# Kernel optimization log

Hardware: AMD Instinct MI355X
Metric: run time of the kernel (lower is better)

The kernel has to match this reference:

```python
import jax, jax.numpy as jnp
import numpy as np
import math

N_HEADS = 16
FACTOR = 5
EPS = 1e-5


def layernorm(x, g, b):
    m = x.mean(-1, keepdims=True)
    v = x.var(-1, keepdims=True)
    return (x - m) / jnp.sqrt(v + EPS) * g + b


def prob_attention(Q, K, V, mask_flag, key):
    # Q: [B, L_Q, H, D], K/V: [B, L_K, H, D] -> internal [B, H, L, D] (Informer ProbAttention)
    Q = Q.transpose(0, 2, 1, 3)
    K = K.transpose(0, 2, 1, 3)
    V = V.transpose(0, 2, 1, 3)
    B, H, L_Q, D = Q.shape
    L_K = K.shape[2]
    U_part = min(FACTOR * int(np.ceil(np.log(L_K))), L_K)  # sampled keys per query
    u = min(FACTOR * int(np.ceil(np.log(L_Q))), L_Q)       # number of active queries
    # sample U_part key indices per query (shared over B, H as in Informer)
    idx = jax.random.randint(key, (L_Q, U_part), 0, L_K)
    K_s = K[:, :, idx, :]                                   # [B,H,L_Q,U_part,D]
    QKs = jnp.einsum('bhld,bhlsd->bhls', Q, K_s)            # sampled scores
    M = QKs.max(-1) - QKs.sum(-1) / L_K                     # sparsity measurement [B,H,L_Q]
    M_top = jax.lax.top_k(M, u)[1]                          # [B,H,u] active query indices
    Q_r = jnp.take_along_axis(Q, M_top[..., None], axis=2)  # [B,H,u,D]
    scale = 1.0 / math.sqrt(D)
    scores = jnp.einsum('bhud,bhkd->bhuk', Q_r, K) * scale  # [B,H,u,L_K]
    if mask_flag:
        # causal mask relative to each selected query's position
        causal = jnp.arange(L_K)[None, None, None, :] > M_top[..., None]
        scores = jnp.where(causal, -jnp.inf, scores)
        context = jnp.cumsum(V, axis=2)                     # initial context for masked case
    else:
        context = jnp.broadcast_to(V.mean(axis=2, keepdims=True), (B, H, L_Q, D))
    attn = jax.nn.softmax(scores, axis=-1)
    ctx = jnp.einsum('bhuk,bhkd->bhud', attn, V)            # [B,H,u,D]
    bi = jnp.arange(B)[:, None, None]
    hi = jnp.arange(H)[None, :, None]
    context = context.at[bi, hi, M_top].set(ctx)            # scatter active queries
    return context.transpose(0, 2, 1, 3)                    # [B,L_Q,H,D]


def mha(x, kv, Wq, bq, Wk, bk, Wv, bv, Wo, bo, mask_flag, key):
    B, L, Dm = x.shape
    Lc = kv.shape[1]
    Dh = Dm // N_HEADS
    Q = (x @ Wq + bq).reshape(B, L, N_HEADS, Dh)
    K = (kv @ Wk + bk).reshape(B, Lc, N_HEADS, Dh)
    V = (kv @ Wv + bv).reshape(B, Lc, N_HEADS, Dh)
    out = prob_attention(Q, K, V, mask_flag, key).reshape(B, L, Dm)
    return out @ Wo + bo


def forward(x, enc_out, sa_Wq, sa_bq, sa_Wk, sa_bk, sa_Wv, sa_bv, sa_Wo, sa_bo,
            ca_Wq, ca_bq, ca_Wk, ca_bk, ca_Wv, ca_bv, ca_Wo, ca_bo,
            ln1_g, ln1_b, ln2_g, ln2_b, ln3_g, ln3_b, ff_W1, ff_b1, ff_W2, ff_b2):
    k1, k2 = jax.random.split(jax.random.key(42))
    x2 = mha(x, x, sa_Wq, sa_bq, sa_Wk, sa_bk, sa_Wv, sa_bv, sa_Wo, sa_bo, True, k1)
    x = layernorm(x + x2, ln1_g, ln1_b)
    x2 = mha(x, enc_out, ca_Wq, ca_bq, ca_Wk, ca_bk, ca_Wv, ca_bv, ca_Wo, ca_bo, False, k2)
    x = layernorm(x + x2, ln2_g, ln2_b)
    x2 = (jax.nn.relu(x @ ff_W1 + ff_b1)) @ ff_W2 + ff_b2
    return layernorm(x + x2, ln3_g, ln3_b)


def setup_inputs() -> dict:
    key = jax.random.key(0)
    D, F = 1024, 4096
    B, L = 4, 1024
    ks = jax.random.split(key, 16)
    s = 0.02
    inp = {
        'x': jax.random.normal(ks[0], (B, L, D), jnp.float32),
        'enc_out': jax.random.normal(ks[1], (B, L, D), jnp.float32),
    }
    names = ['sa_Wq', 'sa_Wk', 'sa_Wv', 'sa_Wo', 'ca_Wq', 'ca_Wk', 'ca_Wv', 'ca_Wo']
    for i, n in enumerate(names):
        inp[n] = jax.random.normal(ks[2 + i], (D, D), jnp.float32) * s
        inp[n.replace('W', 'b')] = jnp.zeros((D,), jnp.float32)
    inp['ff_W1'] = jax.random.normal(ks[10], (D, F), jnp.float32) * s
    inp['ff_b1'] = jnp.zeros((F,), jnp.float32)
    inp['ff_W2'] = jax.random.normal(ks[11], (F, D), jnp.float32) * s
    inp['ff_b2'] = jnp.zeros((D,), jnp.float32)
    for i in (1, 2, 3):
        inp[f'ln{i}_g'] = jnp.ones((D,), jnp.float32)
        inp[f'ln{i}_b'] = jnp.zeros((D,), jnp.float32)
    return inp


def reference(x, enc_out, sa_Wq, sa_bq, sa_Wk, sa_bk, sa_Wv, sa_bv, sa_Wo, sa_bo,
              ca_Wq, ca_bq, ca_Wk, ca_bk, ca_Wv, ca_bv, ca_Wo, ca_bo,
              ln1_g, ln1_b, ln2_g, ln2_b, ln3_g, ln3_b, ff_W1, ff_b1, ff_W2, ff_b2):
    return forward(x, enc_out, sa_Wq, sa_bq, sa_Wk, sa_bk, sa_Wv, sa_bv, sa_Wo, sa_bo,
                   ca_Wq, ca_bq, ca_Wk, ca_bk, ca_Wv, ca_bv, ca_Wo, ca_bo,
                   ln1_g, ln1_b, ln2_g, ln2_b, ln3_g, ln3_b, ff_W1, ff_b1, ff_W2, ff_b2)
```

## Files before the change

kernel.cpp:

```cpp
#include <hip/hip_runtime.h>
#include <cstdint>
#include <cstddef>

#define B_     4
#define L_     1024
#define DM_    1024
#define H_     16
#define DH_    64
#define U_     35
#define FF_    4096
#define MROWS_ 4096
#define IDXN_  35840
#define KS_    4
#define KSP_   16

typedef __attribute__((ext_vector_type(8))) short bf16x8;
typedef __attribute__((ext_vector_type(4))) float f32x4;

__host__ __device__ inline void tf2x32(uint32_t k0, uint32_t k1,
                                       uint32_t x0, uint32_t x1,
                                       uint32_t& y0, uint32_t& y1) {
  const uint32_t ks2 = k0 ^ k1 ^ 0x1BD11BDAu;
  uint32_t v0 = x0 + k0, v1 = x1 + k1;
#define ROTL_(x,d) (((x)<<(d))|((x)>>(32-(d))))
#define RND_(r) { v0 += v1; v1 = ROTL_(v1,(r)); v1 ^= v0; }
  RND_(13) RND_(15) RND_(26) RND_(6)   v0 += k1;  v1 += ks2 + 1u;
  RND_(17) RND_(29) RND_(16) RND_(24)  v0 += ks2; v1 += k0  + 2u;
  RND_(13) RND_(15) RND_(26) RND_(6)   v0 += k0;  v1 += k1  + 3u;
  RND_(17) RND_(29) RND_(16) RND_(24)  v0 += k1;  v1 += ks2 + 4u;
  RND_(13) RND_(15) RND_(26) RND_(6)   v0 += ks2; v1 += k0  + 5u;
#undef RND_
#undef ROTL_
  y0 = v0; y1 = v1;
}

__global__ void idx_kernel(uint32_t k0, uint32_t k1, int* __restrict__ idx) {
  const int i = blockIdx.x * 256 + threadIdx.x;
  if (i >= IDXN_) return;
  uint32_t y0, y1;
  tf2x32(k0, k1, 0u, (uint32_t)i, y0, y1);
  idx[i] = (int)((y0 ^ y1) & 1023u);
}

__device__ __forceinline__ uint32_t f32bits(float x) {
  union { float f; uint32_t u; } c; c.f = x; return c.u;
}
__device__ __forceinline__ float bitsf32(uint32_t u) {
  union { uint32_t u; float f; } c; c.u = u; return c.f;
}
__device__ __forceinline__ uint32_t bf16rne(float x) {
  const uint32_t u = f32bits(x);
  return (u + 0x7FFFu + ((u >> 16) & 1u)) >> 16;
}
__device__ __forceinline__ float bf16tof(uint32_t h) { return bitsf32(h << 16); }

__device__ __forceinline__ void split3(float x, uint32_t& h, uint32_t& m, uint32_t& l) {
  h = bf16rne(x); const float r  = x - bf16tof(h);
  m = bf16rne(r); const float r2 = r - bf16tof(m);
  l = bf16rne(r2);
}

__device__ __forceinline__ void gload16(const void* g, void* l) {
  __builtin_amdgcn_global_load_lds(
      (const __attribute__((address_space(1))) void*)g,
      (__attribute__((address_space(3))) void*)l, 16, 0, 0);
}

template<int LIMBS>
__global__ __launch_bounds__(256) void tsplit_kernel(
    const float* __restrict__ W, short* __restrict__ Th,
    short* __restrict__ Tm, short* __restrict__ Tl, int K, int N)
{
  __shared__ float tile[64][65];
  const int n0 = blockIdx.x * 64, k0 = blockIdx.y * 64;
  const int t = threadIdx.x;
  const int r = t >> 2, c0 = (t & 3) * 16;
  const float* src = W + (size_t)(k0 + r) * N + n0 + c0;
  const float4 v0 = *(const float4*)src;
  const float4 v1 = *(const float4*)(src + 4);
  const float4 v2 = *(const float4*)(src + 8);
  const float4 v3 = *(const float4*)(src + 12);
  float* tr = &tile[r][c0];
  tr[0]=v0.x; tr[1]=v0.y; tr[2]=v0.z; tr[3]=v0.w;
  tr[4]=v1.x; tr[5]=v1.y; tr[6]=v1.z; tr[7]=v1.w;
  tr[8]=v2.x; tr[9]=v2.y; tr[10]=v2.z; tr[11]=v2.w;
  tr[12]=v3.x; tr[13]=v3.y; tr[14]=v3.z; tr[15]=v3.w;
  __syncthreads();
  uint32_t ph[8], pm[8], pl[8];
#pragma unroll
  for (int j = 0; j < 16; j += 2) {
    uint32_t h0,m0,l0,h1,m1,l1;
    split3(tile[c0 + j][r], h0, m0, l0);
    split3(tile[c0 + j + 1][r], h1, m1, l1);
    ph[j>>1] = h0 | (h1 << 16);
    pm[j>>1] = m0 | (m1 << 16);
    pl[j>>1] = l0 | (l1 << 16);
  }
  const size_t ob = (size_t)(n0 + r) * K + k0 + c0;
  *(uint4*)(Th + ob)     = make_uint4(ph[0], ph[1], ph[2], ph[3]);
  *(uint4*)(Th + ob + 8) = make_uint4(ph[4], ph[5], ph[6], ph[7]);
  if (LIMBS == 3) {
    *(uint4*)(Tm + ob)     = make_uint4(pm[0], pm[1], pm[2], pm[3]);
    *(uint4*)(Tm + ob + 8) = make_uint4(pm[4], pm[5], pm[6], pm[7]);
    *(uint4*)(Tl + ob)     = make_uint4(pl[0], pl[1], pl[2], pl[3]);
    *(uint4*)(Tl + ob + 8) = make_uint4(pl[4], pl[5], pl[6], pl[7]);
  }
}

template<int LIMBS>
__global__ void rsplit_kernel(const float* __restrict__ X, short* __restrict__ Th,
                              short* __restrict__ Tm, short* __restrict__ Tl, int n8)
{
  const int i = blockIdx.x * 256 + threadIdx.x;
  if (i >= n8) return;
  const float4 a = ((const float4*)X)[2*i], b = ((const float4*)X)[2*i+1];
  const float v[8] = {a.x,a.y,a.z,a.w,b.x,b.y,b.z,b.w};
  uint32_t ph[4], pm[4], pl[4];
#pragma unroll
  for (int j = 0; j < 4; ++j) {
    uint32_t h0,m0,l0,h1,m1,l1;
    split3(v[2*j], h0, m0, l0);
    split3(v[2*j+1], h1, m1, l1);
    ph[j] = h0 | (h1 << 16); pm[j] = m0 | (m1 << 16); pl[j] = l0 | (l1 << 16);
  }
  ((uint4*)Th)[i] = make_uint4(ph[0], ph[1], ph[2], ph[3]);
  if (LIMBS == 3) {
    ((uint4*)Tm)[i] = make_uint4(pm[0], pm[1], pm[2], pm[3]);
    ((uint4*)Tl)[i] = make_uint4(pl[0], pl[1], pl[2], pl[3]);
  }
}

struct FJob {
  const short* A[3];
  const short* B[3];
  const float* bias;
  float* C;
  short* Ch;
  int relu;
};
struct FJobs { FJob j[3]; };

template<int NL>
__global__ __launch_bounds__(256, 2) void gemm_fused(FJobs jobs, int K, int N)
{
  __shared__ short As[NL][4096] __attribute__((aligned(16)));
  __shared__ short Bs[NL][4096] __attribute__((aligned(16)));
  const int z = blockIdx.z;
  const int nwg  = gridDim.x * gridDim.y;
  const int flat = blockIdx.y * gridDim.x + blockIdx.x;
  const int swz  = (flat & 7) * (nwg >> 3) + (flat >> 3);
  const int bn = (swz % gridDim.x) * 128;
  const int bm = (swz / gridDim.x) * 128;

  const int t = threadIdx.x, lane = t & 63;
  const int wid = t >> 6, wr = wid >> 1, wc = wid & 1;
  const int l15 = lane & 15, kg = lane >> 4;
  const int srow = t >> 2;
  const int sc   = ((t & 3) ^ ((srow + (srow >> 2)) & 3)) * 8;

  int aoff[4], boff[4];
#pragma unroll
  for (int m = 0; m < 4; ++m) {
    const int ra = wr * 64 + m * 16 + l15;
    aoff[m] = ra * 32 + ((kg ^ ((ra + (ra >> 2)) & 3)) << 3);
    const int rb = wc * 64 + m * 16 + l15;
    boff[m] = rb * 32 + ((kg ^ ((rb + (rb >> 2)) & 3)) << 3);
  }

  f32x4 acc[4][4];
#pragma unroll
  for (int m = 0; m < 4; ++m)
#pragma unroll
    for (int n = 0; n < 4; ++n) acc[m][n] = (f32x4){0.f,0.f,0.f,0.f};

  const size_t aofs0 = (size_t)(bm + srow) * K + sc;
  const size_t bofs0 = (size_t)(bn + srow) * K + sc;
  const size_t half  = (size_t)64 * K;

  for (int kk = 0; kk < K; kk += 32) {
    __syncthreads();
#pragma unroll
    for (int l = 0; l < NL; ++l) {
      gload16(jobs.j[z].A[l] + aofs0 + kk,        &As[l][t * 8]);
      gload16(jobs.j[z].A[l] + aofs0 + half + kk, &As[l][2048 + t * 8]);
      gload16(jobs.j[z].B[l] + bofs0 + kk,        &Bs[l][t * 8]);
      gload16(jobs.j[z].B[l] + bofs0 + half + kk, &Bs[l][2048 + t * 8]);
    }
    __syncthreads();
    if (NL == 1) {
      bf16x8 a[4], b[4];
#pragma unroll
      for (int m = 0; m < 4; ++m) a[m] = *(const bf16x8*)&As[0][aoff[m]];
#pragma unroll
      for (int n = 0; n < 4; ++n) b[n] = *(const bf16x8*)&Bs[0][boff[n]];
#pragma unroll
      for (int m = 0; m < 4; ++m)
#pragma unroll
        for (int n = 0; n < 4; ++n)
          acc[m][n] = __builtin_amdgcn_mfma_f32_16x16x32_bf16(a[m], b[n], acc[m][n], 0, 0, 0);
    } else {
      bf16x8 a0[4], a1[4], a2[4], b[4];
#pragma unroll
      for (int m = 0; m < 4; ++m) {
        a0[m] = *(const bf16x8*)&As[0][aoff[m]];
        a1[m] = *(const bf16x8*)&As[1][aoff[m]];
        a2[m] = *(const bf16x8*)&As[2][aoff[m]];
      }
#pragma unroll
      for (int n = 0; n < 4; ++n) b[n] = *(const bf16x8*)&Bs[0][boff[n]];
#pragma unroll
      for (int m = 0; m < 4; ++m)
#pragma unroll
        for (int n = 0; n < 4; ++n) {
          acc[m][n] = __builtin_amdgcn_mfma_f32_16x16x32_bf16(a0[m], b[n], acc[m][n], 0, 0, 0);
          acc[m][n] = __builtin_amdgcn_mfma_f32_16x16x32_bf16(a1[m], b[n], acc[m][n], 0, 0, 0);
          acc[m][n] = __builtin_amdgcn_mfma_f32_16x16x32_bf16(a2[m], b[n], acc[m][n], 0, 0, 0);
        }
#pragma unroll
      for (int n = 0; n < 4; ++n) b[n] = *(const bf16x8*)&Bs[1][boff[n]];
#pragma unroll
      for (int m = 0; m < 4; ++m)
#pragma unroll
        for (int n = 0; n < 4; ++n) {
          acc[m][n] = __builtin_amdgcn_mfma_f32_16x16x32_bf16(a0[m], b[n], acc[m][n], 0, 0, 0);
          acc[m][n] = __builtin_amdgcn_mfma_f32_16x16x32_bf16(a1[m], b[n], acc[m][n], 0, 0, 0);
        }
#pragma unroll
      for (int n = 0; n < 4; ++n) b[n] = *(const bf16x8*)&Bs[2][boff[n]];
#pragma unroll
      for (int m = 0; m < 4; ++m)
#pragma unroll
        for (int n = 0; n < 4; ++n)
          acc[m][n] = __builtin_amdgcn_mfma_f32_16x16x32_bf16(a0[m], b[n], acc[m][n], 0, 0, 0);
    }
  }

  const float* bias = jobs.j[z].bias;
  float* C  = jobs.j[z].C;
  short* Ch = jobs.j[z].Ch;
  const int relu = jobs.j[z].relu;
  float bv[4];
#pragma unroll
  for (int n = 0; n < 4; ++n) bv[n] = bias[bn + wc*64 + n*16 + l15];
#pragma unroll
  for (int m = 0; m < 4; ++m) {
    const int row0 = bm + wr*64 + m*16 + kg*4;
#pragma unroll
    for (int n = 0; n < 4; ++n) {
      const int col = bn + wc*64 + n*16 + l15;
#pragma unroll
      for (int q = 0; q < 4; ++q) {
        float o = acc[m][n][q] + bv[n];
        if (relu) o = fmaxf(o, 0.f);
        const size_t off = (size_t)(row0 + q) * N + col;
        if (C)  C[off]  = o;
        if (Ch) Ch[off] = (short)bf16rne(o);
      }
    }
  }
}

__global__ __launch_bounds__(256, 2) void qks_m_kernel(
    const float* __restrict__ Q, const float* __restrict__ K,
    const int* __restrict__ idx, float* __restrict__ Mout)
{
  __shared__ int sidx[64 * U_];
  const int p = blockIdx.x;
  const int g  = (p & 7) + (((p >> 3) & 7) << 3);
  const int q16 = p >> 6;
  const int l0 = q16 * 64;
  const int tid = threadIdx.x;
  for (int i = tid; i < 64 * U_; i += 256) sidx[i] = idx[l0 * U_ + i];
  __syncthreads();

  const int ll = tid >> 2, dq = tid & 3;
  const int l = l0 + ll;
  const int h = g & (H_ - 1), b = g >> 4;
  const size_t rowb = (size_t)(b * L_) * DM_ + h * DH_;
  const float* qrow = Q + rowb + (size_t)l * DM_ + dq * 4;
  float4 qv[4];
#pragma unroll
  for (int jj = 0; jj < 4; ++jj) qv[jj] = *(const float4*)(qrow + jj * 16);

  const int* ip = &sidx[ll * U_];
  float mx = -__builtin_inff();
  float sm = 0.f;
#pragma unroll 5
  for (int s = 0; s < U_; ++s) {
    const float* krow = K + rowb + (size_t)ip[s] * DM_ + dq * 4;
    const float4 k0 = *(const float4*)(krow);
    const float4 k1 = *(const float4*)(krow + 16);
    const float4 k2 = *(const float4*)(krow + 32);
    const float4 k3 = *(const float4*)(krow + 48);
    float a0 = 0.f, a1 = 0.f, a2 = 0.f, a3 = 0.f;
    a0 = fmaf(qv[0].x, k0.x, a0); a0 = fmaf(qv[0].y, k0.y, a0);
    a0 = fmaf(qv[0].z, k0.z, a0); a0 = fmaf(qv[0].w, k0.w, a0);
    a1 = fmaf(qv[1].x, k1.x, a1); a1 = fmaf(qv[1].y, k1.y, a1);
    a1 = fmaf(qv[1].z, k1.z, a1); a1 = fmaf(qv[1].w, k1.w, a1);
    a2 = fmaf(qv[2].x, k2.x, a2); a2 = fmaf(qv[2].y, k2.y, a2);
    a2 = fmaf(qv[2].z, k2.z, a2); a2 = fmaf(qv[2].w, k2.w, a2);
    a3 = fmaf(qv[3].x, k3.x, a3); a3 = fmaf(qv[3].y, k3.y, a3);
    a3 = fmaf(qv[3].z, k3.z, a3); a3 = fmaf(qv[3].w, k3.w, a3);
    float a = (a0 + a1) + (a2 + a3);
    a += __shfl_xor(a, 1, 64);
    a += __shfl_xor(a, 2, 64);
    mx = fmaxf(mx, a);
    sm += a;
  }
  if (dq == 0) Mout[g * L_ + l] = mx - sm * (1.0f / 1024.0f);
}

__global__ __launch_bounds__(256) void topk_kernel(
    const float* __restrict__ M, int* __restrict__ Mtop)
{
  const int bh  = blockIdx.x;
  const int tid = threadIdx.x;
  __shared__ float vals[L_];
  __shared__ float rv[256];
  __shared__ int   ri[256];
  for (int i = tid; i < L_; i += 256) vals[i] = M[(size_t)bh * L_ + i];
  __syncthreads();
  for (int t = 0; t < U_; ++t) {
    float best = -__builtin_inff();
    int   bi   = L_;
    for (int i = tid; i < L_; i += 256) {
      const float v = vals[i];
      if (v > best) { best = v; bi = i; }
    }
    rv[tid] = best; ri[tid] = bi;
    __syncthreads();
    for (int s = 128; s > 0; s >>= 1) {
      if (tid < s) {
        if (rv[tid+s] > rv[tid] || (rv[tid+s] == rv[tid] && ri[tid+s] < ri[tid])) {
          rv[tid] = rv[tid+s]; ri[tid] = ri[tid+s];
        }
      }
      __syncthreads();
    }
    if (tid == 0) { Mtop[bh * U_ + t] = ri[0]; vals[ri[0]] = -__builtin_inff(); }
    __syncthreads();
  }
}

template<int UBASE, int UCNT>
__device__ __forceinline__ void score_group(
    const float* __restrict__ kp, const float* qs, const int* rowsL,
    uint32_t* __restrict__ prow, const int k, const int masked)
{
  float s[UCNT];
#pragma unroll
  for (int ug = 0; ug < UCNT; ++ug) s[ug] = 0.f;
#pragma unroll
  for (int dc = 0; dc < 64; dc += 16) {
    const float4 k0 = *(const float4*)(kp + dc);
    const float4 k1 = *(const float4*)(kp + dc + 4);
    const float4 k2 = *(const float4*)(kp + dc + 8);
    const float4 k3 = *(const float4*)(kp + dc + 12);
#pragma unroll
    for (int ug = 0; ug < UCNT; ++ug) {
      const float4* qp = (const float4*)&qs[(UBASE + ug) * 64 + dc];
      const float4 q0 = qp[0], q1 = qp[1], q2 = qp[2], q3 = qp[3];
      float acc = s[ug];
      acc = fmaf(q0.x, k0.x, acc); acc = fmaf(q0.y, k0.y, acc);
      acc = fmaf(q0.z, k0.z, acc); acc = fmaf(q0.w, k0.w, acc);
      acc = fmaf(q1.x, k1.x, acc); acc = fmaf(q1.y, k1.y, acc);
      acc = fmaf(q1.z, k1.z, acc); acc = fmaf(q1.w, k1.w, acc);
      acc = fmaf(q2.x, k2.x, acc); acc = fmaf(q2.y, k2.y, acc);
      acc = fmaf(q2.z, k2.z, acc); acc = fmaf(q2.w, k2.w, acc);
      acc = fmaf(q3.x, k3.x, acc); acc = fmaf(q3.y, k3.y, acc);
      acc = fmaf(q3.z, k3.z, acc); acc = fmaf(q3.w, k3.w, acc);
      s[ug] = acc;
    }
  }
#pragma unroll
  for (int ug = 0; ug < UCNT; ++ug) {
    float v = s[ug] * 0.125f;
    if (masked && k > rowsL[UBASE + ug]) v = -__builtin_inff();
    s[ug] = expf(v);
  }
#pragma unroll
  for (int j = 0; j < UCNT / 2; ++j)
    prow[UBASE / 2 + j] = bf16rne(s[2 * j]) | (bf16rne(s[2 * j + 1]) << 16);
  if (UCNT & 1)
    prow[UBASE / 2 + UCNT / 2] = bf16rne(s[UCNT - 1]);
}

__global__ __launch_bounds__(256) void attn_score(
    const float* __restrict__ Q, const float* __restrict__ K,
    const int* __restrict__ Mtop, uint32_t* __restrict__ Pg, int masked)
{
  __shared__ float qs[U_ * DH_];
  __shared__ int   rowsL[U_ + 1];
  const int bh = blockIdx.x >> 2, ks = blockIdx.x & 3;
  const int h = bh & (H_ - 1), b = bh >> 4;
  const int tid = threadIdx.x;
  const size_t kvbase = (size_t)(b * L_) * DM_ + h * DH_;

  if (tid < U_) rowsL[tid] = Mtop[bh * U_ + tid];
  __syncthreads();
  for (int i = tid; i < U_ * DH_; i += 256)
    qs[i] = Q[kvbase + (size_t)rowsL[i >> 6] * DM_ + (i & 63)];
  __syncthreads();

  const int k = ks * 256 + tid;
  const float* kp = K + kvbase + (size_t)k * DM_;
  uint32_t* prow = Pg + (size_t)bh * (L_ * 18) + (size_t)k * 18;
  score_group<0, 12>(kp, qs, rowsL, prow, k, masked);
  score_group<12, 12>(kp, qs, rowsL, prow, k, masked);
  score_group<24, 11>(kp, qs, rowsL, prow, k, masked);
}

__global__ __launch_bounds__(256) void attn_pv(
    const float* __restrict__ V, const uint32_t* __restrict__ Pg,
    float* __restrict__ Opart, float* __restrict__ Dpart)
{
  __shared__ uint32_t Pl[64 * 18];
  const int p = blockIdx.x;
  const int xcd = p & 7, idx2 = p >> 3;
  const int bh = xcd + ((idx2 & 7) << 3);
  const int ks = idx2 >> 3;
  const int h = bh & (H_ - 1), b = bh >> 4;
  const int tid = threadIdx.x, lane = tid & 63, wid = tid >> 6;
  const size_t kvbase = (size_t)(b * L_) * DM_ + h * DH_;

  const uint32_t* ps = Pg + (size_t)bh * (L_ * 18) + (size_t)(ks * 64) * 18;
  for (int i = tid; i < 64 * 18; i += 256) Pl[i] = ps[i];
  __syncthreads();

  float acc[9], dd[9];
#pragma unroll
  for (int j = 0; j < 9; ++j) { acc[j] = 0.f; dd[j] = 0.f; }

  const float* vp = V + kvbase + (size_t)(ks * 64) * DM_ + lane;
  const int widh = wid >> 1;
  const int hi   = wid & 1;
#pragma unroll 8
  for (int kk = 0; kk < 64; ++kk) {
    const float v0 = vp[(size_t)kk * DM_];
    const uint32_t* pr = &Pl[kk * 18];
#pragma unroll
    for (int j = 0; j < 9; ++j) {
      if (wid + 4 * j < U_) {
        const uint32_t w = pr[widh + 2 * j];
        const float p2 = hi ? bitsf32(w & 0xFFFF0000u) : bitsf32(w << 16);
        acc[j] = fmaf(p2, v0, acc[j]);
        dd[j] += p2;
      }
    }
  }
  const int pb = (ks * 64 + bh) * U_;
#pragma unroll
  for (int j = 0; j < 9; ++j) {
    const int u = wid + 4 * j;
    if (u < U_) {
      Opart[(size_t)(pb + u) * 64 + lane] = acc[j];
      if (lane == 0) Dpart[pb + u] = dd[j];
    }
  }
}

__global__ void attn_reduce(const float* __restrict__ Opart,
                            const float* __restrict__ Dpart,
                            float* __restrict__ ctx_rows)
{
  const int bhu = blockIdx.x;
  const int bh = bhu / U_, u = bhu % U_;
  const int lane = threadIdx.x;
  float o = 0.f, dd = 0.f;
#pragma unroll
  for (int ks = 0; ks < KSP_; ++ks) {
    o  += Opart[(size_t)((ks * 64 + bh) * U_ + u) * 64 + lane];
    dd += Dpart[(ks * 64 + bh) * U_ + u];
  }
  ctx_rows[(size_t)bhu * 64 + lane] = o / dd;
}

__global__ __launch_bounds__(256) void cumsum_kernel(
    const float* __restrict__ V, float* __restrict__ C)
{
  const int bh = blockIdx.x;
  const int h = bh & (H_ - 1), b = bh >> 4;
  const int d = threadIdx.x & 63, qq = threadIdx.x >> 6;
  __shared__ float chs[4][DH_];
  const size_t base = (size_t)b * L_ * DM_ + h * DH_ + d;
  float acc = 0.f;
  const int l0 = qq * 256;
  for (int l = l0; l < l0 + 256; ++l) acc += V[base + (size_t)l * DM_];
  chs[qq][d] = acc;
  __syncthreads();
  float off = 0.f;
  for (int j = 0; j < qq; ++j) off += chs[j][d];
  acc = off;
  for (int l = l0; l < l0 + 256; ++l) {
    acc += V[base + (size_t)l * DM_];
    C[base + (size_t)l * DM_] = acc;
  }
}

__global__ __launch_bounds__(256) void vmean_kernel(
    const float* __restrict__ V, float* __restrict__ vm)
{
  const int bh = blockIdx.x;
  const int h = bh & (H_ - 1), b = bh >> 4;
  const int d = threadIdx.x & 63, qq = threadIdx.x >> 6;
  __shared__ float chs[4][DH_];
  const size_t base = (size_t)b * L_ * DM_ + h * DH_ + d;
  float acc = 0.f;
  for (int l = qq * 256; l < qq * 256 + 256; ++l) acc += V[base + (size_t)l * DM_];
  chs[qq][d] = acc;
  __syncthreads();
  if (qq == 0)
    vm[bh * DH_ + d] = (chs[0][d] + chs[1][d] + chs[2][d] + chs[3][d]) * (1.0f / 1024.0f);
}

__global__ void fill_kernel(const float* __restrict__ vm, float* __restrict__ C)
{
  const size_t i = (size_t)blockIdx.x * 256 + threadIdx.x;
  const int d = (int)(i & 63);
  const int h = (int)((i >> 6) & (H_ - 1));
  const int b = (int)(i >> 20);
  C[i] = vm[(b * H_ + h) * DH_ + d];
}

__global__ void scatter_kernel(const float* __restrict__ ctx_rows,
                               const int* __restrict__ Mtop, float* __restrict__ C)
{
  const int bhu = blockIdx.x;
  const int u  = bhu % U_;
  const int bh = bhu / U_;
  const int h = bh & (H_ - 1), b = bh >> 4;
  const int row = Mtop[bh * U_ + u];
  C[(size_t)(b * L_ + row) * DM_ + h * DH_ + threadIdx.x] =
      ctx_rows[(size_t)bhu * DH_ + threadIdx.x];
}

__global__ __launch_bounds__(256) void ln_kernel(
    const float* __restrict__ xa, const float* __restrict__ xb,
    const float* __restrict__ g, const float* __restrict__ bt,
    float* __restrict__ out, short* __restrict__ oh,
    short* __restrict__ om, short* __restrict__ ol)
{
  const int row = blockIdx.x;
  const int tid = threadIdx.x;
  __shared__ float v[DM_];
  __shared__ float red[256];
  float s = 0.f;
  for (int i = tid; i < DM_; i += 256) {
    const float t = xa[(size_t)row * DM_ + i] + xb[(size_t)row * DM_ + i];
    v[i] = t; s += t;
  }
  red[tid] = s; __syncthreads();
  for (int st = 128; st > 0; st >>= 1) { if (tid < st) red[tid] += red[tid+st]; __syncthreads(); }
  const float mean = red[0] * (1.0f / DM_);
  __syncthreads();
  float s2 = 0.f;
  for (int i = tid; i < DM_; i += 256) { const float dd = v[i] - mean; s2 += dd * dd; }
  red[tid] = s2; __syncthreads();
  for (int st = 128; st > 0; st >>= 1) { if (tid < st) red[tid] += red[tid+st]; __syncthreads(); }
  const float rstd = rsqrtf(red[0] * (1.0f / DM_) + 1e-5f);
  __syncthreads();
  for (int i = tid; i < DM_; i += 256) {
    const size_t idx = (size_t)row * DM_ + i;
    const float o = (v[i] - mean) * rstd * g[i] + bt[i];
    out[idx] = o;
    if (oh) {
      const uint32_t h = bf16rne(o);
      oh[idx] = (short)h;
      if (om) {
        const float r = o - bf16tof(h);
        const uint32_t m = bf16rne(r);
        om[idx] = (short)m;
        ol[idx] = (short)bf16rne(r - bf16tof(m));
      }
    }
  }
}

extern "C" void kernel_launch(void* const* d_in, const int* in_sizes, int n_in,
                              void* d_out, int out_size, void* d_ws, size_t ws_size,
                              hipStream_t stream)
{
  (void)in_sizes; (void)n_in; (void)out_size; (void)ws_size;
  const float* x    = (const float*)d_in[0];
  const float* enc  = (const float*)d_in[1];
  const float* saWq = (const float*)d_in[2];  const float* sabq = (const float*)d_in[3];
  const float* saWk = (const float*)d_in[4];  const float* sabk = (const float*)d_in[5];
  const float* saWv = (const float*)d_in[6];  const float* sabv = (const float*)d_in[7];
  const float* saWo = (const float*)d_in[8];  const float* sabo = (const float*)d_in[9];
  const float* caWq = (const float*)d_in[10]; const float* cabq = (const float*)d_in[11];
  const float* caWk = (const float*)d_in[12]; const float* cabk = (const float*)d_in[13];
  const float* caWv = (const float*)d_in[14]; const float* cabv = (const float*)d_in[15];
  const float* caWo = (const float*)d_in[16]; const float* cabo = (const float*)d_in[17];
  const float* fW1  = (const float*)d_in[18]; const float* fb1  = (const float*)d_in[19];
  const float* fW2  = (const float*)d_in[20]; const float* fb2  = (const float*)d_in[21];
  const float* l1g  = (const float*)d_in[22]; const float* l1b  = (const float*)d_in[23];
  const float* l2g  = (const float*)d_in[24]; const float* l2b  = (const float*)d_in[25];
  const float* l3g  = (const float*)d_in[26]; const float* l3b  = (const float*)d_in[27];

  float* ws = (float*)d_ws;
  const size_t SL = (size_t)MROWS_ * DM_;
  float* bufQ = ws;
  float* bufK = ws + SL;
  float* bufV = ws + 2 * SL;
  float* bufC = ws + 3 * SL;
  float* xcur = ws + 4 * SL;
  float* tmp  = ws + 5 * SL;
  float* smallp = ws + 6 * SL;
  int*   idxb = (int*)smallp;
  float* Mbuf = smallp + 36864;
  int*   Mtop = (int*)(smallp + 36864 + 65536);
  float* ctxr = smallp + 36864 + 65536 + 2304;
  float* vm   = ctxr + 143360;

  uint32_t* Pg    = (uint32_t*)bufC;
  float*    Opart = bufC + 1179648;
  float*    Dpart = Opart + (size_t)KSP_ * 64 * U_ * 64;

  const size_t M1 = 1024u * 1024u;
  short* wreg = (short*)(ws + 6 * SL + 262144);
  short* areg = wreg + 8 * M1;
  short* Wqh = wreg;          short* Wqm = wreg + 1*M1; short* Wql = wreg + 2*M1;
  short* Wkh = wreg + 3*M1;   short* Wkm = wreg + 4*M1; short* Wkl = wreg + 5*M1;
  short* Wvh = wreg + 6*M1;   short* Woh = wreg + 7*M1;
  short* f1h = wreg;          short* f2h = wreg + 4*M1;
  short* xh = areg;           short* xm = areg + 4*M1;  short* xl = areg + 8*M1;
  short* eh = areg + 12*M1;   short* em = areg + 16*M1; short* el = areg + 20*M1;
  short* bCh = areg + 12*M1;
  short* hidh = (short*)bufQ;

  uint32_t k1a, k1b, k2a, k2b;
  tf2x32(0u, 42u, 0u, 0u, k1a, k1b);
  tf2x32(0u, 42u, 0u, 1u, k2a, k2b);
  uint32_t kb1a, kb1b, kb2a, kb2b;
  tf2x32(k1a, k1b, 0u, 1u, kb1a, kb1b);
  tf2x32(k2a, k2b, 0u, 1u, kb2a, kb2b);

  const dim3 thr(256);
  const int gIdx = (IDXN_ + 255) / 256;
  const int n8 = (int)(SL / 8);
  const dim3 gT(16, 16);

  tsplit_kernel<3><<<gT, thr, 0, stream>>>(saWq, Wqh, Wqm, Wql, DM_, DM_);
  tsplit_kernel<3><<<gT, thr, 0, stream>>>(saWk, Wkh, Wkm, Wkl, DM_, DM_);
  tsplit_kernel<1><<<gT, thr, 0, stream>>>(saWv, Wvh, nullptr, nullptr, DM_, DM_);
  tsplit_kernel<1><<<gT, thr, 0, stream>>>(saWo, Woh, nullptr, nullptr, DM_, DM_);
  rsplit_kernel<3><<<n8 / 256, thr, 0, stream>>>(x, xh, xm, xl, n8);
  {
    FJobs J = {};
    J.j[0] = { {xh, xm, xl}, {Wqh, Wqm, Wql}, sabq, bufQ, nullptr, 0 };
    J.j[1] = { {xh, xm, xl}, {Wkh, Wkm, Wkl}, sabk, bufK, nullptr, 0 };
    gemm_fused<3><<<dim3(8, 32, 2), thr, 0, stream>>>(J, DM_, DM_);
  }
  {
    FJobs J = {};
    J.j[0] = { {xh, nullptr, nullptr}, {Wvh, nullptr, nullptr}, sabv, bufV, nullptr, 0 };
    gemm_fused<1><<<dim3(8, 32, 1), thr, 0, stream>>>(J, DM_, DM_);
  }
  idx_kernel<<<gIdx, thr, 0, stream>>>(kb1a, kb1b, idxb);
  qks_m_kernel<<<1024, thr, 0, stream>>>(bufQ, bufK, idxb, Mbuf);
  topk_kernel<<<B_ * H_, thr, 0, stream>>>(Mbuf, Mtop);
  attn_score<<<B_ * H_ * KS_, thr, 0, stream>>>(bufQ, bufK, Mtop, Pg, 1);
  attn_pv<<<B_ * H_ * KSP_, thr, 0, stream>>>(bufV, Pg, Opart, Dpart);
  attn_reduce<<<B_ * H_ * U_, dim3(64), 0, stream>>>(Opart, Dpart, ctxr);
  cumsum_kernel<<<B_ * H_, thr, 0, stream>>>(bufV, bufC);
  scatter_kernel<<<B_ * H_ * U_, dim3(64), 0, stream>>>(ctxr, Mtop, bufC);
  rsplit_kernel<1><<<n8 / 256, thr, 0, stream>>>(bufC, bCh, nullptr, nullptr, n8);
  {
    FJobs J = {};
    J.j[0] = { {bCh, nullptr, nullptr}, {Woh, nullptr, nullptr}, sabo, tmp, nullptr, 0 };
    gemm_fused<1><<<dim3(8, 32, 1), thr, 0, stream>>>(J, DM_, DM_);
  }
  ln_kernel<<<MROWS_, thr, 0, stream>>>(x, tmp, l1g, l1b, xcur, xh, xm, xl);

  tsplit_kernel<3><<<gT, thr, 0, stream>>>(caWq, Wqh, Wqm, Wql, DM_, DM_);
  tsplit_kernel<3><<<gT, thr, 0, stream>>>(caWk, Wkh, Wkm, Wkl, DM_, DM_);
  tsplit_kernel<1><<<gT, thr, 0, stream>>>(caWv, Wvh, nullptr, nullptr, DM_, DM_);
  tsplit_kernel<1><<<gT, thr, 0, stream>>>(caWo, Woh, nullptr, nullptr, DM_, DM_);
  rsplit_kernel<3><<<n8 / 256, thr, 0, stream>>>(enc, eh, em, el, n8);
  {
    FJobs J = {};
    J.j[0] = { {xh, xm, xl}, {Wqh, Wqm, Wql}, cabq, bufQ, nullptr, 0 };
    J.j[1] = { {eh, em, el}, {Wkh, Wkm, Wkl}, cabk, bufK, nullptr, 0 };
    gemm_fused<3><<<dim3(8, 32, 2), thr, 0, stream>>>(J, DM_, DM_);
  }
  {
    FJobs J = {};
    J.j[0] = { {eh, nullptr, nullptr}, {Wvh, nullptr, nullptr}, cabv, bufV, nullptr, 0 };
    gemm_fused<1><<<dim3(8, 32, 1), thr, 0, stream>>>(J, DM_, DM_);
  }
  idx_kernel<<<gIdx, thr, 0, stream>>>(kb2a, kb2b, idxb);
  qks_m_kernel<<<1024, thr, 0, stream>>>(bufQ, bufK, idxb, Mbuf);
  topk_kernel<<<B_ * H_, thr, 0, stream>>>(Mbuf, Mtop);
  attn_score<<<B_ * H_ * KS_, thr, 0, stream>>>(bufQ, bufK, Mtop, Pg, 0);
  attn_pv<<<B_ * H_ * KSP_, thr, 0, stream>>>(bufV, Pg, Opart, Dpart);
  attn_reduce<<<B_ * H_ * U_, dim3(64), 0, stream>>>(Opart, Dpart, ctxr);
  vmean_kernel<<<B_ * H_, thr, 0, stream>>>(bufV, vm);
  fill_kernel<<<(int)(SL / 256), thr, 0, stream>>>(vm, bufC);
  scatter_kernel<<<B_ * H_ * U_, dim3(64), 0, stream>>>(ctxr, Mtop, bufC);
  rsplit_kernel<1><<<n8 / 256, thr, 0, stream>>>(bufC, bCh, nullptr, nullptr, n8);
  {
    FJobs J = {};
    J.j[0] = { {bCh, nullptr, nullptr}, {Woh, nullptr, nullptr}, cabo, tmp, nullptr, 0 };
    gemm_fused<1><<<dim3(8, 32, 1), thr, 0, stream>>>(J, DM_, DM_);
  }
  ln_kernel<<<MROWS_, thr, 0, stream>>>(xcur, tmp, l2g, l2b, xcur, xh, nullptr, nullptr);

  tsplit_kernel<1><<<dim3(64, 16), thr, 0, stream>>>(fW1, f1h, nullptr, nullptr, DM_, FF_);
  tsplit_kernel<1><<<dim3(16, 64), thr, 0, stream>>>(fW2, f2h, nullptr, nullptr, FF_, DM_);
  {
    FJobs J = {};
    J.j[0] = { {xh, nullptr, nullptr}, {f1h, nullptr, nullptr}, fb1, nullptr, hidh, 1 };
    gemm_fused<1><<<dim3(32, 32, 1), thr, 0, stream>>>(J, DM_, FF_);
  }
  {
    FJobs J = {};
    J.j[0] = { {hidh, nullptr, nullptr}, {f2h, nullptr, nullptr}, fb2, tmp, nullptr, 0 };
    gemm_fused<1><<<dim3(8, 32, 1), thr, 0, stream>>>(J, FF_, DM_);
  }
  ln_kernel<<<MROWS_, thr, 0, stream>>>(xcur, tmp, l3g, l3b, (float*)d_out,
                                        nullptr, nullptr, nullptr);
}
```

Before: 793.1 us.

## Split attn_score dot products across 4 lanes per key with shuffle reduction

The attn_score kernel now assigns four threads to each key row, each handling a 16-element slice of the head dimension, and combines the partial dots with xor shuffles before exp and bf16 packing. The grid grows from 4 to 16 key splits per (batch, head), with an XCD-aware block-to-head mapping, so there are more blocks and less serial work per thread. This targets the small grid and long per-thread serial loop of the old version, at the cost of redundant exp work across the four lanes and shuffle overhead. Separately, the GEMM launch bound is raised to 3 blocks per CU, which tightens the register budget and may cause spills.

```diff
diff --git a/kernel.cpp b/kernel.cpp
--- a/kernel.cpp
+++ b/kernel.cpp
@@ -11,7 +11,7 @@
 #define FF_    4096
 #define MROWS_ 4096
 #define IDXN_  35840
-#define KS_    4
+#define KSC_   16
 #define KSP_   16
 
 typedef __attribute__((ext_vector_type(8))) short bf16x8;
@@ -141,7 +141,7 @@
 struct FJobs { FJob j[3]; };
 
 template<int NL>
-__global__ __launch_bounds__(256, 2) void gemm_fused(FJobs jobs, int K, int N)
+__global__ __launch_bounds__(256, 3) void gemm_fused(FJobs jobs, int K, int N)
 {
   __shared__ short As[NL][4096] __attribute__((aligned(16)));
   __shared__ short Bs[NL][4096] __attribute__((aligned(16)));
@@ -342,56 +342,16 @@
   }
 }
 
-template<int UBASE, int UCNT>
-__device__ __forceinline__ void score_group(
-    const float* __restrict__ kp, const float* qs, const int* rowsL,
-    uint32_t* __restrict__ prow, const int k, const int masked)
-{
-  float s[UCNT];
-#pragma unroll
-  for (int ug = 0; ug < UCNT; ++ug) s[ug] = 0.f;
-#pragma unroll
-  for (int dc = 0; dc < 64; dc += 16) {
-    const float4 k0 = *(const float4*)(kp + dc);
-    const float4 k1 = *(const float4*)(kp + dc + 4);
-    const float4 k2 = *(const float4*)(kp + dc + 8);
-    const float4 k3 = *(const float4*)(kp + dc + 12);
-#pragma unroll
-    for (int ug = 0; ug < UCNT; ++ug) {
-      const float4* qp = (const float4*)&qs[(UBASE + ug) * 64 + dc];
-      const float4 q0 = qp[0], q1 = qp[1], q2 = qp[2], q3 = qp[3];
-      float acc = s[ug];
-      acc = fmaf(q0.x, k0.x, acc); acc = fmaf(q0.y, k0.y, acc);
-      acc = fmaf(q0.z, k0.z, acc); acc = fmaf(q0.w, k0.w, acc);
-      acc = fmaf(q1.x, k1.x, acc); acc = fmaf(q1.y, k1.y, acc);
-      acc = fmaf(q1.z, k1.z, acc); acc = fmaf(q1.w, k1.w, acc);
-      acc = fmaf(q2.x, k2.x, acc); acc = fmaf(q2.y, k2.y, acc);
-      acc = fmaf(q2.z, k2.z, acc); acc = fmaf(q2.w, k2.w, acc);
-      acc = fmaf(q3.x, k3.x, acc); acc = fmaf(q3.y, k3.y, acc);
-      acc = fmaf(q3.z, k3.z, acc); acc = fmaf(q3.w, k3.w, acc);
-      s[ug] = acc;
-    }
-  }
-#pragma unroll
-  for (int ug = 0; ug < UCNT; ++ug) {
-    float v = s[ug] * 0.125f;
-    if (masked && k > rowsL[UBASE + ug]) v = -__builtin_inff();
-    s[ug] = expf(v);
-  }
-#pragma unroll
-  for (int j = 0; j < UCNT / 2; ++j)
-    prow[UBASE / 2 + j] = bf16rne(s[2 * j]) | (bf16rne(s[2 * j + 1]) << 16);
-  if (UCNT & 1)
-    prow[UBASE / 2 + UCNT / 2] = bf16rne(s[UCNT - 1]);
-}
-
 __global__ __launch_bounds__(256) void attn_score(
     const float* __restrict__ Q, const float* __restrict__ K,
     const int* __restrict__ Mtop, uint32_t* __restrict__ Pg, int masked)
 {
   __shared__ float qs[U_ * DH_];
   __shared__ int   rowsL[U_ + 1];
-  const int bh = blockIdx.x >> 2, ks = blockIdx.x & 3;
+  const int p = blockIdx.x;
+  const int xcd = p & 7, idx2 = p >> 3;
+  const int bh = xcd + ((idx2 & 7) << 3);
+  const int ks = idx2 >> 3;
   const int h = bh & (H_ - 1), b = bh >> 4;
   const int tid = threadIdx.x;
   const size_t kvbase = (size_t)(b * L_) * DM_ + h * DH_;
@@ -402,12 +362,55 @@
     qs[i] = Q[kvbase + (size_t)rowsL[i >> 6] * DM_ + (i & 63)];
   __syncthreads();
 
-  const int k = ks * 256 + tid;
-  const float* kp = K + kvbase + (size_t)k * DM_;
-  uint32_t* prow = Pg + (size_t)bh * (L_ * 18) + (size_t)k * 18;
-  score_group<0, 12>(kp, qs, rowsL, prow, k, masked);
-  score_group<12, 12>(kp, qs, rowsL, prow, k, masked);
-  score_group<24, 11>(kp, qs, rowsL, prow, k, masked);
+  const int grp = tid >> 2, dq = tid & 3;
+  const int k = ks * 64 + grp;
+  const float* kp = K + kvbase + (size_t)k * DM_ + dq * 16;
+  const float4 kv0 = *(const float4*)(kp);
+  const float4 kv1 = *(const float4*)(kp + 4);
+  const float4 kv2 = *(const float4*)(kp + 8);
+  const float4 kv3 = *(const float4*)(kp + 12);
+
+#define DOT_EXP_U(uu, out)                                                  \
+  {                                                                         \
+    const float4* qp = (const float4*)&qs[(uu) * 64 + dq * 16];             \
+    const float4 q0 = qp[0], q1 = qp[1], q2 = qp[2], q3 = qp[3];            \
+    float x0 = 0.f, x1 = 0.f;                                               \
+    x0 = fmaf(q0.x, kv0.x, x0); x0 = fmaf(q0.y, kv0.y, x0);                 \
+    x0 = fmaf(q0.z, kv0.z, x0); x0 = fmaf(q0.w, kv0.w, x0);                 \
+    x1 = fmaf(q1.x, kv1.x, x1); x1 = fmaf(q1.y, kv1.y, x1);                 \
+    x1 = fmaf(q1.z, kv1.z, x1); x1 = fmaf(q1.w, kv1.w, x1);                 \
+    x0 = fmaf(q2.x, kv2.x, x0); x0 = fmaf(q2.y, kv2.y, x0);                 \
+    x0 = fmaf(q2.z, kv2.z, x0); x0 = fmaf(q2.w, kv2.w, x0);                 \
+    x1 = fmaf(q3.x, kv3.x, x1); x1 = fmaf(q3.y, kv3.y, x1);                 \
+    x1 = fmaf(q3.z, kv3.z, x1); x1 = fmaf(q3.w, kv3.w, x1);                 \
+    float a = x0 + x1;                                                      \
+    a += __shfl_xor(a, 1, 64);                                              \
+    a += __shfl_xor(a, 2, 64);                                              \
+    float v = a * 0.125f;                                                   \
+    if (masked && k > rowsL[(uu)]) v = -__builtin_inff();                   \
+    out = expf(v);                                                          \
+  }
+
+  uint32_t pk[18];
+#pragma unroll
+  for (int j = 0; j < 17; ++j) {
+    float e0, e1;
+    DOT_EXP_U(2 * j, e0);
+    DOT_EXP_U(2 * j + 1, e1);
+    pk[j] = bf16rne(e0) | (bf16rne(e1) << 16);
+  }
+  {
+    float e;
+    DOT_EXP_U(34, e);
+    pk[17] = bf16rne(e);
+  }
+#undef DOT_EXP_U
+
+  if (dq == 0) {
+    uint32_t* prow = Pg + (size_t)bh * (L_ * 18) + (size_t)k * 18;
+#pragma unroll
+    for (int j = 0; j < 18; ++j) prow[j] = pk[j];
+  }
 }
 
 __global__ __launch_bounds__(256) void attn_pv(
@@ -659,7 +662,7 @@
   idx_kernel<<<gIdx, thr, 0, stream>>>(kb1a, kb1b, idxb);
   qks_m_kernel<<<1024, thr, 0, stream>>>(bufQ, bufK, idxb, Mbuf);
   topk_kernel<<<B_ * H_, thr, 0, stream>>>(Mbuf, Mtop);
-  attn_score<<<B_ * H_ * KS_, thr, 0, stream>>>(bufQ, bufK, Mtop, Pg, 1);
+  attn_score<<<B_ * H_ * KSC_, thr, 0, stream>>>(bufQ, bufK, Mtop, Pg, 1);
   attn_pv<<<B_ * H_ * KSP_, thr, 0, stream>>>(bufV, Pg, Opart, Dpart);
   attn_reduce<<<B_ * H_ * U_, dim3(64), 0, stream>>>(Opart, Dpart, ctxr);
   cumsum_kernel<<<B_ * H_, thr, 0, stream>>>(bufV, bufC);
@@ -691,7 +694,7 @@
   idx_kernel<<<gIdx, thr, 0, stream>>>(kb2a, kb2b, idxb);
   qks_m_kernel<<<1024, thr, 0, stream>>>(bufQ, bufK, idxb, Mbuf);
   topk_kernel<<<B_ * H_, thr, 0, stream>>>(Mbuf, Mtop);
-  attn_score<<<B_ * H_ * KS_, thr, 0, stream>>>(bufQ, bufK, Mtop, Pg, 0);
+  attn_score<<<B_ * H_ * KSC_, thr, 0, stream>>>(bufQ, bufK, Mtop, Pg, 0);
   attn_pv<<<B_ * H_ * KSP_, thr, 0, stream>>>(bufV, Pg, Opart, Dpart);
   attn_reduce<<<B_ * H_ * U_, dim3(64), 0, stream>>>(Opart, Dpart, ctxr);
   vmean_kernel<<<B_ * H_, thr, 0, stream>>>(bufV, vm);
```

Result: no change. 787.8 us (-0.7%).
